# Performance work log

Hardware: AMD Instinct MI355X
Metric: run time of the kernel (lower is better)

## Reference

```python
import jax, jax.numpy as jnp
import numpy as np

IN_FEATURES = 5000
N0, N1, N2 = 512, 512, 256   # num_nodes; encoder: in->N0->N2 (skips N1), decoder: N2->N1->N0->2*in
NUM_TREATMENTS = 20
BATCH = 8192
TREAT_COLS = 2


def _glorot(key, shape):
    fan_in, fan_out = shape[-2], shape[-1]
    lim = np.sqrt(6.0 / (fan_in + fan_out)).astype(np.float32)
    return jax.random.uniform(key, shape, jnp.float32, -lim, lim)


def setup_inputs() -> dict:
    key = jax.random.key(0)
    ks = jax.random.split(key, 12)
    inp = {
        "input": jax.random.normal(ks[0], (BATCH, IN_FEATURES), jnp.float32),
        "treatment": jax.random.randint(ks[1], (BATCH, TREAT_COLS), 0, NUM_TREATMENTS + 1),
        # encoder: in -> N0 -> N2 (both layers ReLU)
        "enc_W1": _glorot(ks[2], (IN_FEATURES, N0)),
        "enc_b1": jnp.zeros((N0,), jnp.float32),
        "enc_W2": _glorot(ks[3], (N0, N2)),
        "enc_b2": jnp.zeros((N2,), jnp.float32),
        # per-treatment single layers: N2 -> N2, ReLU
        "T_W": _glorot(ks[4], (NUM_TREATMENTS, N2, N2)),
        "T_b": jnp.zeros((NUM_TREATMENTS, N2), jnp.float32),
        # decoder: N2 -> N1 -> N0 -> 2*in (last layer linear)
        "dec_W1": _glorot(ks[5], (N2, N1)),
        "dec_b1": jnp.zeros((N1,), jnp.float32),
        "dec_W2": _glorot(ks[6], (N1, N0)),
        "dec_b2": jnp.zeros((N0,), jnp.float32),
        "dec_W3": _glorot(ks[7], (N0, 2 * IN_FEATURES)),
        "dec_b3": jnp.zeros((2 * IN_FEATURES,), jnp.float32),
    }
    return inp


def reference(input, treatment, enc_W1, enc_b1, enc_W2, enc_b2, T_W, T_b,
              dec_W1, dec_b1, dec_W2, dec_b2, dec_W3, dec_b3):
    dim = input.shape[1]
    # encoder
    h = jax.nn.relu(input @ enc_W1 + enc_b1)
    embedding = jax.nn.relu(h @ enc_W2 + enc_b2)            # [B, N2]

    # per-treatment dispatch, vectorized over experts
    tvals = jnp.arange(1, NUM_TREATMENTS + 1)               # treatments are 1-indexed
    mask = jnp.any(treatment[None, :, :] == tvals[:, None, None], axis=-1)  # [T, B] bool
    # original skips a treatment unless more than one sample is assigned to it
    apply_t = jnp.sum(mask, axis=1) > 1                     # [T]
    gate = (mask & apply_t[:, None]).astype(embedding.dtype)  # [T, B]

    expert_out = jax.nn.relu(jnp.einsum('bd,tde->tbe', embedding, T_W) + T_b[:, None, :])  # [T, B, N2]
    latent_rep = jnp.einsum('tbe,tb->be', expert_out, gate)  # scatter-add of masked experts

    # decoder
    h = jax.nn.relu(latent_rep @ dec_W1 + dec_b1)
    h = jax.nn.relu(h @ dec_W2 + dec_b2)
    rec = h @ dec_W3 + dec_b3                               # [B, 2*dim]

    gene_means = rec[:, :dim]
    gene_vars = jax.nn.softplus(rec[:, dim:]) + 0.001
    return jnp.concatenate([gene_means, gene_vars], axis=1)
```

## Files before the change

kernel.cpp:

```cpp
#include <hip/hip_runtime.h>
#include <hip/hip_bf16.h>
#include <hip/hip_fp16.h>
#include <math.h>

#define BATCH 8192
#define IN_F 5000
#define KP1 5024
#define NN0 512
#define NN1 512
#define NN2 256
#define NTREAT 20
#define OUTF (2*IN_F)
#define NP3 10240

typedef _Float16 f16;
typedef _Float16 f16x8 __attribute__((ext_vector_type(8)));
typedef float f32x4 __attribute__((ext_vector_type(4)));
typedef __attribute__((address_space(3))) void as3_void;
typedef const __attribute__((address_space(1))) void cas1_void;

__device__ __forceinline__ int fswz(int row) { return (row >> 1) & 3; }

__device__ __forceinline__ float softplusf(float x) {
    return fmaxf(x, 0.f) + log1pf(expf(-fabsf(x)));
}

__global__ void zero64_kernel(int* __restrict__ p) {
    if (threadIdx.x < 64) p[threadIdx.x] = 0;
}
__global__ void count_kernel(const int* __restrict__ treat, int* __restrict__ cnt) {
    int b = blockIdx.x * blockDim.x + threadIdx.x;
    if (b >= BATCH) return;
    int t0 = treat[2*b], t1 = treat[2*b+1];
    if (t0 >= 1 && t0 <= NTREAT) atomicAdd(&cnt[t0], 1);
    if (t1 >= 1 && t1 <= NTREAT && t1 != t0) atomicAdd(&cnt[t1], 1);
}
__global__ void pair_kernel(const int* __restrict__ treat, const int* __restrict__ cnt,
                            int* __restrict__ epair) {
    int b = blockIdx.x * blockDim.x + threadIdx.x;
    if (b >= BATCH) return;
    int t0 = treat[2*b], t1 = treat[2*b+1];
    int e0 = (t0 >= 1 && t0 <= NTREAT && cnt[t0] > 1) ? (t0 - 1) : -1;
    int e1 = (t1 >= 1 && t1 <= NTREAT && t1 != t0 && cnt[t1] > 1) ? (t1 - 1) : -1;
    epair[2*b] = e0;
    epair[2*b+1] = e1;
}
__global__ void scatter_kernel(const int* __restrict__ epair, int* __restrict__ pos,
                               int* __restrict__ rows) {
    int b = blockIdx.x * blockDim.x + threadIdx.x;
    if (b >= BATCH) return;
    #pragma unroll
    for (int p = 0; p < 2; ++p) {
        int t = epair[2*b + p];
        if (t >= 0) {
            int x = atomicAdd(&pos[t], 1);
            rows[t * BATCH + x] = b * 2 + p;
        }
    }
}

__global__ __launch_bounds__(256) void convw_kernel(
    const float* __restrict__ W, f16* __restrict__ Whi, f16* __restrict__ Wlo,
    int K, int N, int Kp) {
    __shared__ float t[64][65];
    const int k0 = blockIdx.x * 64;
    const int n0 = blockIdx.y * 64;
    const int tid = threadIdx.x;
    #pragma unroll
    for (int i = 0; i < 16; ++i) {
        int idx = tid + i*256;
        int r = idx >> 6, c = idx & 63;
        float v = 0.f;
        if (k0 + r < K && n0 + c < N) v = W[(size_t)(k0+r)*N + n0 + c];
        t[r][c] = v;
    }
    __syncthreads();
    const int n = tid >> 2;
    const int q0 = (tid & 3) * 2;
    const int f = fswz(n0 + n);
    #pragma unroll
    for (int h = 0; h < 2; ++h) {
        int q = q0 + h;
        if (k0 + q*8 >= Kp) continue;
        f16x8 hv, lv;
        #pragma unroll
        for (int j = 0; j < 8; ++j) {
            float x = t[q*8 + j][n];
            f16 hi = (f16)x;
            hv[j] = hi;
            lv[j] = (f16)(x - (float)hi);
        }
        size_t base = (size_t)(n0 + n) * Kp + (size_t)(k0 + (((q & 3) ^ f) << 3) + (q >> 2) * 32);
        *(f16x8*)&Whi[base] = hv;
        *(f16x8*)&Wlo[base] = lv;
    }
}

__global__ __launch_bounds__(256) void expert_gemm(
    const float* __restrict__ emb, const float* __restrict__ T_W,
    const float* __restrict__ T_b, const int* __restrict__ pos,
    const int* __restrict__ rows, float* __restrict__ latA, float* __restrict__ latB) {
    const int t = blockIdx.x;
    const int n = pos[t];
    const int base = blockIdx.y * 16;
    if (base >= n) return;
    const int nr = min(16, n - base);
    __shared__ float se[16][256];
    __shared__ int ridx[16];
    const int tid = threadIdx.x;
    if (tid < 16) ridx[tid] = (tid < nr) ? rows[t * BATCH + base + tid] : 0;
    __syncthreads();
    #pragma unroll
    for (int s = 0; s < 16; ++s)
        se[s][tid] = (s < nr) ? emb[(size_t)(ridx[s] >> 1) * NN2 + tid] : 0.f;
    __syncthreads();
    float acc[16];
    const float bcol = T_b[t * NN2 + tid];
    #pragma unroll
    for (int s = 0; s < 16; ++s) acc[s] = bcol;
    const float* W = T_W + (size_t)t * NN2 * NN2 + tid;
    for (int d0 = 0; d0 < NN2; d0 += 4) {
        float w0 = W[(size_t)(d0+0) * NN2];
        float w1 = W[(size_t)(d0+1) * NN2];
        float w2 = W[(size_t)(d0+2) * NN2];
        float w3 = W[(size_t)(d0+3) * NN2];
        #pragma unroll
        for (int s = 0; s < 16; ++s) {
            float4 e = *(const float4*)&se[s][d0];
            acc[s] = fmaf(e.x, w0, fmaf(e.y, w1, fmaf(e.z, w2, fmaf(e.w, w3, acc[s]))));
        }
    }
    for (int s = 0; s < nr; ++s) {
        int rp = ridx[s];
        float* dst = (rp & 1) ? latB : latA;
        dst[(size_t)(rp >> 1) * NN2 + tid] = fmaxf(acc[s], 0.f);
    }
}

__global__ __launch_bounds__(256) void latconv_kernel(
    const float* __restrict__ latA, const float* __restrict__ latB,
    f16* __restrict__ lhi, f16* __restrict__ llo) {
    const int idx = blockIdx.x * 256 + threadIdx.x;
    const int m = idx >> 8, k = idx & 255;
    float v = latA[idx] + latB[idx];
    f16 hi = (f16)v;
    size_t o = (size_t)m * NN2 + (size_t)(k ^ (fswz(m) << 3));
    lhi[o] = hi;
    llo[o] = (f16)(v - (float)hi);
}

template<int MODE, bool XCVT, int BN, int BM = 256>
__global__ __launch_bounds__((BM == 128) ? 256 : 512, 2) void gemm8(
    const f16* __restrict__ Xhi, const f16* __restrict__ Xlo,
    const float* __restrict__ X32, int ldx,
    const f16* __restrict__ Whi, const f16* __restrict__ Wlo,
    const float* __restrict__ bias,
    float* __restrict__ C32, f16* __restrict__ Chi, f16* __restrict__ Clo,
    int Kp, int K_real, int N_real, int NpOut, int halfN) {
    constexpr int NTH = (BM == 128) ? 256 : 512;
    constexpr int NWAVE = NTH / 64;
    constexpr int WN_WAVES = (BN == 256) ? 4 : 2;
    constexpr int WM_WAVES = NWAVE / WN_WAVES;
    constexpr int WMT = BM / WM_WAVES;
    constexpr int WNT = BN / WN_WAVES;
    constexpr int MF = WMT / 16;
    constexpr int NF = WNT / 16;
    constexpr int XSZ = BM * 32;
    constexpr int WSZ = BN * 32;
    __shared__ f16 lds[2][2*XSZ + 2*WSZ];

    const int tid = threadIdx.x;
    const int wid = tid >> 6;
    const int lane = tid & 63;
    const int lr = lane & 15;
    const int ls = lane >> 4;
    const int m0 = blockIdx.y * BM;
    const int n0 = blockIdx.x * BN;
    const int wm = (wid / WN_WAVES) * WMT;
    const int wn = (wid % WN_WAVES) * WNT;
    const int koff = ((ls ^ ((lr >> 1) & 3)) << 3);
    const int nk = Kp / 32;

    f32x4 acc[MF][NF] = {};

    auto stage = [&](int bi, int kt) {
        f16* Xh = lds[bi];
        f16* Xl = Xh + XSZ;
        f16* Wh = Xl + XSZ;
        f16* Wl = Wh + WSZ;
        const int kk = kt * 32 + (lane & 3) * 8;
        const int rlo = lane >> 2;
        if constexpr (BN == 256) {
            #pragma unroll
            for (int c = 0; c < 2; ++c) {
                const int rb = c * 128 + wid * 16;
                const size_t g = (size_t)(n0 + rb + rlo) * Kp + kk;
                __builtin_amdgcn_global_load_lds((cas1_void*)(Whi + g), (as3_void*)(Wh + rb*32), 16, 0, 0);
                __builtin_amdgcn_global_load_lds((cas1_void*)(Wlo + g), (as3_void*)(Wl + rb*32), 16, 0, 0);
            }
        } else if constexpr (BN == 128) {
            #pragma unroll
            for (int c = 0; c < 2; ++c) {
                const int rb = wid * 32 + c * 16;
                const size_t g = (size_t)(n0 + rb + rlo) * Kp + kk;
                __builtin_amdgcn_global_load_lds((cas1_void*)(Whi + g), (as3_void*)(Wh + rb*32), 16, 0, 0);
                __builtin_amdgcn_global_load_lds((cas1_void*)(Wlo + g), (as3_void*)(Wl + rb*32), 16, 0, 0);
            }
        } else {
            const int rb = (wid & 3) * 16;
            const size_t g = (size_t)(n0 + rb + rlo) * Kp + kk;
            const f16* src = (wid < 4) ? (Whi + g) : (Wlo + g);
            f16* dst = ((wid < 4) ? Wh : Wl) + rb*32;
            __builtin_amdgcn_global_load_lds((cas1_void*)src, (as3_void*)dst, 16, 0, 0);
        }
        if constexpr (!XCVT) {
            if constexpr (BM == 256) {
                #pragma unroll
                for (int c = 0; c < 2; ++c) {
                    const int rb = c * 128 + wid * 16;
                    const size_t g = (size_t)(m0 + rb + rlo) * Kp + kk;
                    __builtin_amdgcn_global_load_lds((cas1_void*)(Xhi + g), (as3_void*)(Xh + rb*32), 16, 0, 0);
                    __builtin_amdgcn_global_load_lds((cas1_void*)(Xlo + g), (as3_void*)(Xl + rb*32), 16, 0, 0);
                }
            } else {
                #pragma unroll
                for (int c = 0; c < 2; ++c) {
                    const int rb = wid * 32 + c * 16;
                    const size_t g = (size_t)(m0 + rb + rlo) * Kp + kk;
                    __builtin_amdgcn_global_load_lds((cas1_void*)(Xhi + g), (as3_void*)(Xh + rb*32), 16, 0, 0);
                    __builtin_amdgcn_global_load_lds((cas1_void*)(Xlo + g), (as3_void*)(Xl + rb*32), 16, 0, 0);
                }
            }
        } else {
            const int ar = tid >> 1;
            const int q0 = (tid & 1) * 2;
            const int fr = fswz(ar);
            const int k0 = kt * 32;
            const float* ap = X32 + (size_t)(m0 + ar) * ldx + (size_t)(k0 + q0 * 8);
            float v[16];
            if (k0 + 32 <= K_real) {
                float4 u0 = *(const float4*)(ap);
                float4 u1 = *(const float4*)(ap + 4);
                float4 u2 = *(const float4*)(ap + 8);
                float4 u3 = *(const float4*)(ap + 12);
                v[0]=u0.x; v[1]=u0.y; v[2]=u0.z; v[3]=u0.w;
                v[4]=u1.x; v[5]=u1.y; v[6]=u1.z; v[7]=u1.w;
                v[8]=u2.x; v[9]=u2.y; v[10]=u2.z; v[11]=u2.w;
                v[12]=u3.x; v[13]=u3.y; v[14]=u3.z; v[15]=u3.w;
            } else {
                #pragma unroll
                for (int j2 = 0; j2 < 16; ++j2) {
                    int kk2 = k0 + q0*8 + j2;
                    v[j2] = (kk2 < K_real) ? X32[(size_t)(m0 + ar) * ldx + kk2] : 0.f;
                }
            }
            #pragma unroll
            for (int h2 = 0; h2 < 2; ++h2) {
                f16x8 hv, lv;
                #pragma unroll
                for (int j2 = 0; j2 < 8; ++j2) {
                    float x = v[h2*8 + j2];
                    f16 hh = (f16)x;
                    hv[j2] = hh;
                    lv[j2] = (f16)(x - (float)hh);
                }
                const int dst = ar*32 + (((q0 + h2) ^ fr) << 3);
                *(f16x8*)&Xh[dst] = hv;
                *(f16x8*)&Xl[dst] = lv;
            }
        }
    };

    stage(0, 0);
    __syncthreads();
    for (int t = 0; t < nk; ++t) {
        if (t + 1 < nk) stage((t + 1) & 1, t + 1);
        const f16* Xh = lds[t & 1];
        const f16* Xl = Xh + XSZ;
        const f16* Wh = Xl + XSZ;
        const f16* Wl = Wh + WSZ;
        f16x8 bh[NF], bl[NF];
        #pragma unroll
        for (int j = 0; j < NF; ++j) {
            const int r = (wn + j*16 + lr) * 32 + koff;
            bh[j] = *(const f16x8*)&Wh[r];
            bl[j] = *(const f16x8*)&Wl[r];
        }
        __builtin_amdgcn_s_setprio(1);
        #pragma unroll
        for (int ih = 0; ih < MF; ih += 4) {
            f16x8 ah[4], al[4];
            #pragma unroll
            for (int i = 0; i < 4; ++i) {
                const int r = (wm + (ih + i)*16 + lr) * 32 + koff;
                ah[i] = *(const f16x8*)&Xh[r];
                al[i] = *(const f16x8*)&Xl[r];
            }
            #pragma unroll
            for (int i = 0; i < 4; ++i)
                #pragma unroll
                for (int j = 0; j < NF; ++j)
                    acc[ih+i][j] = __builtin_amdgcn_mfma_f32_16x16x32_f16(ah[i], bh[j], acc[ih+i][j], 0, 0, 0);
            #pragma unroll
            for (int i = 0; i < 4; ++i)
                #pragma unroll
                for (int j = 0; j < NF; ++j)
                    acc[ih+i][j] = __builtin_amdgcn_mfma_f32_16x16x32_f16(ah[i], bl[j], acc[ih+i][j], 0, 0, 0);
            #pragma unroll
            for (int i = 0; i < 4; ++i)
                #pragma unroll
                for (int j = 0; j < NF; ++j)
                    acc[ih+i][j] = __builtin_amdgcn_mfma_f32_16x16x32_f16(al[i], bh[j], acc[ih+i][j], 0, 0, 0);
        }
        __builtin_amdgcn_s_setprio(0);
        __syncthreads();
    }

    #pragma unroll
    for (int i = 0; i < MF; ++i) {
        #pragma unroll
        for (int j = 0; j < NF; ++j) {
            const int col = n0 + wn + j*16 + lr;
            if (col >= N_real) continue;
            const float bcol = bias[col];
            #pragma unroll
            for (int q = 0; q < 4; ++q) {
                const int m = m0 + wm + i*16 + ls*4 + q;
                float vv = acc[i][j][q] + bcol;
                if (MODE == 0) {
                    C32[(size_t)m * N_real + col] = fmaxf(vv, 0.f);
                } else if (MODE == 1) {
                    vv = fmaxf(vv, 0.f);
                    f16 hi = (f16)vv;
                    const size_t idx = (size_t)m * NpOut + (size_t)(col ^ (fswz(m) << 3));
                    Chi[idx] = hi;
                    Clo[idx] = (f16)(vv - (float)hi);
                } else {
                    if (col >= halfN) vv = softplusf(vv) + 0.001f;
                    C32[(size_t)m * N_real + col] = vv;
                }
            }
        }
    }
}

extern "C" void kernel_launch(void* const* d_in, const int* in_sizes, int n_in,
                              void* d_out, int out_size, void* d_ws, size_t ws_size,
                              hipStream_t stream) {
    const float* input  = (const float*)d_in[0];
    const int*   treat  = (const int*)d_in[1];
    const float* enc_W1 = (const float*)d_in[2];
    const float* enc_b1 = (const float*)d_in[3];
    const float* enc_W2 = (const float*)d_in[4];
    const float* enc_b2 = (const float*)d_in[5];
    const float* T_W    = (const float*)d_in[6];
    const float* T_b    = (const float*)d_in[7];
    const float* dec_W1 = (const float*)d_in[8];
    const float* dec_b1 = (const float*)d_in[9];
    const float* dec_W2 = (const float*)d_in[10];
    const float* dec_b2 = (const float*)d_in[11];
    const float* dec_W3 = (const float*)d_in[12];
    const float* dec_b3 = (const float*)d_in[13];
    float* out = (float*)d_out;

    uint8_t* p = (uint8_t*)d_ws;
    f16* h1hi = (f16*)p;  float* latA = (float*)p;  p += (size_t)BATCH*NN0*2;
    f16* h1lo = (f16*)p;  float* latB = (float*)p;  p += (size_t)BATCH*NN0*2;
    float* emb = (float*)p;  f16* h4hi = (f16*)p;   p += (size_t)BATCH*NN2*4;
    f16* lathi = (f16*)p;  f16* h4lo = (f16*)p;     p += (size_t)BATCH*NN2*2;
    f16* latlo = (f16*)p;                           p += (size_t)BATCH*NN2*2;
    f16* w1hi = (f16*)p;               p += (size_t)NN0*KP1*2;
    f16* w1lo = (f16*)p;               p += (size_t)NN0*KP1*2;
    f16* w2hi = (f16*)p;               p += (size_t)NN2*NN0*2;
    f16* w2lo = (f16*)p;               p += (size_t)NN2*NN0*2;
    f16* dw1hi = (f16*)p;              p += (size_t)NN1*NN2*2;
    f16* dw1lo = (f16*)p;              p += (size_t)NN1*NN2*2;
    f16* dw2hi = (f16*)p;              p += (size_t)NN0*NN1*2;
    f16* dw2lo = (f16*)p;              p += (size_t)NN0*NN1*2;
    f16* dw3hi = (f16*)p;              p += (size_t)NP3*NN0*2;
    f16* dw3lo = (f16*)p;              p += (size_t)NP3*NN0*2;
    int* cnt   = (int*)p;              p += 32*4;
    int* pos   = (int*)p;              p += 32*4;
    int* epair = (int*)p;              p += (size_t)BATCH*2*4;
    int* rows  = (int*)p;              p += (size_t)NTREAT*BATCH*4;
    f16* h3hi = h1hi;
    f16* h3lo = h1lo;

    zero64_kernel<<<1, 64, 0, stream>>>(cnt);
    count_kernel<<<BATCH/256, 256, 0, stream>>>(treat, cnt);
    pair_kernel<<<BATCH/256, 256, 0, stream>>>(treat, cnt, epair);
    scatter_kernel<<<BATCH/256, 256, 0, stream>>>(epair, pos, rows);

    convw_kernel<<<dim3((KP1+63)/64, NN0/64), 256, 0, stream>>>(enc_W1, w1hi, w1lo, IN_F, NN0, KP1);
    convw_kernel<<<dim3(NN0/64, NN2/64), 256, 0, stream>>>(enc_W2, w2hi, w2lo, NN0, NN2, NN0);
    convw_kernel<<<dim3(NN2/64, NN1/64), 256, 0, stream>>>(dec_W1, dw1hi, dw1lo, NN2, NN1, NN2);
    convw_kernel<<<dim3(NN1/64, NN0/64), 256, 0, stream>>>(dec_W2, dw2hi, dw2lo, NN1, NN0, NN1);
    convw_kernel<<<dim3(NN0/64, NP3/64), 256, 0, stream>>>(dec_W3, dw3hi, dw3lo, NN0, OUTF, NN0);

    gemm8<1, true, 64><<<dim3(NN0/64, BATCH/256), 512, 0, stream>>>(
        nullptr, nullptr, input, IN_F, w1hi, w1lo, enc_b1,
        nullptr, h1hi, h1lo, KP1, IN_F, NN0, NN0, 0);
    gemm8<0, false, 64><<<dim3(NN2/64, BATCH/256), 512, 0, stream>>>(
        h1hi, h1lo, nullptr, 0, w2hi, w2lo, enc_b2,
        emb, nullptr, nullptr, NN0, NN0, NN2, NN2, 0);
    hipMemsetAsync(latA, 0, (size_t)BATCH*NN2*4*2, stream);
    expert_gemm<<<dim3(NTREAT, BATCH/16), 256, 0, stream>>>(emb, T_W, T_b, pos, rows, latA, latB);
    latconv_kernel<<<BATCH*NN2/256, 256, 0, stream>>>(latA, latB, lathi, latlo);
    gemm8<1, false, 64><<<dim3(NN1/64, BATCH/256), 512, 0, stream>>>(
        lathi, latlo, nullptr, 0, dw1hi, dw1lo, dec_b1,
        nullptr, h3hi, h3lo, NN2, NN2, NN1, NN1, 0);
    gemm8<1, false, 64><<<dim3(NN0/64, BATCH/256), 512, 0, stream>>>(
        h3hi, h3lo, nullptr, 0, dw2hi, dw2lo, dec_b2,
        nullptr, h4hi, h4lo, NN1, NN1, NN0, NN0, 0);
    gemm8<2, false, 128, 128><<<dim3(NP3/128, BATCH/128), 256, 0, stream>>>(
        h4hi, h4lo, nullptr, 0, dw3hi, dw3lo, dec_b3,
        out, nullptr, nullptr, NN0, NN0, OUTF, OUTF, IN_F);
}
```

Measured before the change: 946.0 us.

## Prefetch two K-tiles ahead with vmcnt waits in non-converting GEMM path

For the non-XCVT GEMM path, the main loop now issues loads two K-tiles ahead into the double buffer. It waits on a partial vmcnt instead of a full barrier, and reads all A/B fragments into registers before releasing the buffer for the next prefetch. This is meant to hide global-to-LDS latency behind the MFMA work and replace __syncthreads with finer-grained waits. It also removes the BN==256 staging branch. Holding all fragments at once raises register pressure, and the hardcoded vmcnt thresholds depend on the exact per-thread load count.

```diff
diff --git a/kernel.cpp b/kernel.cpp
--- a/kernel.cpp
+++ b/kernel.cpp
@@ -167,6 +167,7 @@
     constexpr int NF = WNT / 16;
     constexpr int XSZ = BM * 32;
     constexpr int WSZ = BN * 32;
+    constexpr int GLL = (BN == 64) ? 5 : 8;
     __shared__ f16 lds[2][2*XSZ + 2*WSZ];
 
     const int tid = threadIdx.x;
@@ -190,15 +191,7 @@
         f16* Wl = Wh + WSZ;
         const int kk = kt * 32 + (lane & 3) * 8;
         const int rlo = lane >> 2;
-        if constexpr (BN == 256) {
-            #pragma unroll
-            for (int c = 0; c < 2; ++c) {
-                const int rb = c * 128 + wid * 16;
-                const size_t g = (size_t)(n0 + rb + rlo) * Kp + kk;
-                __builtin_amdgcn_global_load_lds((cas1_void*)(Whi + g), (as3_void*)(Wh + rb*32), 16, 0, 0);
-                __builtin_amdgcn_global_load_lds((cas1_void*)(Wlo + g), (as3_void*)(Wl + rb*32), 16, 0, 0);
-            }
-        } else if constexpr (BN == 128) {
+        if constexpr (BN == 128) {
             #pragma unroll
             for (int c = 0; c < 2; ++c) {
                 const int rb = wid * 32 + c * 16;
@@ -271,49 +264,100 @@
         }
     };
 
-    stage(0, 0);
-    __syncthreads();
-    for (int t = 0; t < nk; ++t) {
-        if (t + 1 < nk) stage((t + 1) & 1, t + 1);
-        const f16* Xh = lds[t & 1];
-        const f16* Xl = Xh + XSZ;
-        const f16* Wh = Xl + XSZ;
-        const f16* Wl = Wh + WSZ;
-        f16x8 bh[NF], bl[NF];
-        #pragma unroll
-        for (int j = 0; j < NF; ++j) {
-            const int r = (wn + j*16 + lr) * 32 + koff;
-            bh[j] = *(const f16x8*)&Wh[r];
-            bl[j] = *(const f16x8*)&Wl[r];
-        }
-        __builtin_amdgcn_s_setprio(1);
-        #pragma unroll
-        for (int ih = 0; ih < MF; ih += 4) {
-            f16x8 ah[4], al[4];
-            #pragma unroll
-            for (int i = 0; i < 4; ++i) {
-                const int r = (wm + (ih + i)*16 + lr) * 32 + koff;
+    if constexpr (!XCVT) {
+        stage(0, 0);
+        stage(1, 1);
+        for (int t = 0; t < nk; ++t) {
+            if (t + 1 < nk) {
+                asm volatile("s_waitcnt vmcnt(%0)" :: "i"(GLL) : "memory");
+            } else {
+                asm volatile("s_waitcnt vmcnt(0)" ::: "memory");
+            }
+            __builtin_amdgcn_s_barrier();
+            const f16* Xh = lds[t & 1];
+            const f16* Xl = Xh + XSZ;
+            const f16* Wh = Xl + XSZ;
+            const f16* Wl = Wh + WSZ;
+            f16x8 bh[NF], bl[NF], ah[MF], al[MF];
+            #pragma unroll
+            for (int j = 0; j < NF; ++j) {
+                const int r = (wn + j*16 + lr) * 32 + koff;
+                bh[j] = *(const f16x8*)&Wh[r];
+                bl[j] = *(const f16x8*)&Wl[r];
+            }
+            #pragma unroll
+            for (int i = 0; i < MF; ++i) {
+                const int r = (wm + i*16 + lr) * 32 + koff;
                 ah[i] = *(const f16x8*)&Xh[r];
                 al[i] = *(const f16x8*)&Xl[r];
             }
-            #pragma unroll
-            for (int i = 0; i < 4; ++i)
+            asm volatile("s_waitcnt lgkmcnt(0)" ::: "memory");
+            __builtin_amdgcn_sched_barrier(0);
+            __builtin_amdgcn_s_barrier();
+            if (t + 2 < nk) stage(t & 1, t + 2);
+            __builtin_amdgcn_s_setprio(1);
+            #pragma unroll
+            for (int i = 0; i < MF; ++i)
                 #pragma unroll
                 for (int j = 0; j < NF; ++j)
-                    acc[ih+i][j] = __builtin_amdgcn_mfma_f32_16x16x32_f16(ah[i], bh[j], acc[ih+i][j], 0, 0, 0);
-            #pragma unroll
-            for (int i = 0; i < 4; ++i)
+                    acc[i][j] = __builtin_amdgcn_mfma_f32_16x16x32_f16(ah[i], bh[j], acc[i][j], 0, 0, 0);
+            #pragma unroll
+            for (int i = 0; i < MF; ++i)
                 #pragma unroll
                 for (int j = 0; j < NF; ++j)
-                    acc[ih+i][j] = __builtin_amdgcn_mfma_f32_16x16x32_f16(ah[i], bl[j], acc[ih+i][j], 0, 0, 0);
-            #pragma unroll
-            for (int i = 0; i < 4; ++i)
+                    acc[i][j] = __builtin_amdgcn_mfma_f32_16x16x32_f16(ah[i], bl[j], acc[i][j], 0, 0, 0);
+            #pragma unroll
+            for (int i = 0; i < MF; ++i)
                 #pragma unroll
                 for (int j = 0; j < NF; ++j)
-                    acc[ih+i][j] = __builtin_amdgcn_mfma_f32_16x16x32_f16(al[i], bh[j], acc[ih+i][j], 0, 0, 0);
-        }
-        __builtin_amdgcn_s_setprio(0);
+                    acc[i][j] = __builtin_amdgcn_mfma_f32_16x16x32_f16(al[i], bh[j], acc[i][j], 0, 0, 0);
+            __builtin_amdgcn_s_setprio(0);
+        }
+    } else {
+        stage(0, 0);
         __syncthreads();
+        for (int t = 0; t < nk; ++t) {
+            if (t + 1 < nk) stage((t + 1) & 1, t + 1);
+            const f16* Xh = lds[t & 1];
+            const f16* Xl = Xh + XSZ;
+            const f16* Wh = Xl + XSZ;
+            const f16* Wl = Wh + WSZ;
+            f16x8 bh[NF], bl[NF];
+            #pragma unroll
+            for (int j = 0; j < NF; ++j) {
+                const int r = (wn + j*16 + lr) * 32 + koff;
+                bh[j] = *(const f16x8*)&Wh[r];
+                bl[j] = *(const f16x8*)&Wl[r];
+            }
+            __builtin_amdgcn_s_setprio(1);
+            #pragma unroll
+            for (int ih = 0; ih < MF; ih += 4) {
+                f16x8 ah[4], al[4];
+                #pragma unroll
+                for (int i = 0; i < 4; ++i) {
+                    const int r = (wm + (ih + i)*16 + lr) * 32 + koff;
+                    ah[i] = *(const f16x8*)&Xh[r];
+                    al[i] = *(const f16x8*)&Xl[r];
+                }
+                #pragma unroll
+                for (int i = 0; i < 4; ++i)
+                    #pragma unroll
+                    for (int j = 0; j < NF; ++j)
+                        acc[ih+i][j] = __builtin_amdgcn_mfma_f32_16x16x32_f16(ah[i], bh[j], acc[ih+i][j], 0, 0, 0);
+                #pragma unroll
+                for (int i = 0; i < 4; ++i)
+                    #pragma unroll
+                    for (int j = 0; j < NF; ++j)
+                        acc[ih+i][j] = __builtin_amdgcn_mfma_f32_16x16x32_f16(ah[i], bl[j], acc[ih+i][j], 0, 0, 0);
+                #pragma unroll
+                for (int i = 0; i < 4; ++i)
+                    #pragma unroll
+                    for (int j = 0; j < NF; ++j)
+                        acc[ih+i][j] = __builtin_amdgcn_mfma_f32_16x16x32_f16(al[i], bh[j], acc[ih+i][j], 0, 0, 0);
+            }
+            __builtin_amdgcn_s_setprio(0);
+            __syncthreads();
+        }
     }
 
     #pragma unroll
```

After: 932.9 us. About the same (-1.4%).
